# Optimization experiments

Measured on AMD Instinct MI355X. Metric: run time of the kernel, lower is better.

## Reference

```python
import jax, jax.numpy as jnp
import numpy as np

H = 64
N_BENE, N_DIAG, N_TREAT = 200000, 10000, 100000
E = 1000000
N_INST = 500000

def setup_inputs() -> dict:
    key = jax.random.key(0)
    ks = jax.random.split(key, 24)
    def lin(k, din, dout):
        kw, kb = jax.random.split(k)
        s = 1.0 / np.sqrt(din)
        return (jax.random.uniform(kw, (din, dout), jnp.float32, -s, s),
                jax.random.uniform(kb, (dout,), jnp.float32, -s, s))
    inp = {
        'bene_ids': jax.random.randint(ks[0], (N_BENE,), 0, 10000, jnp.int32),
        'diag_ids': jax.random.randint(ks[1], (N_DIAG,), 0, 200, jnp.int32),
        'treatment_ids': jax.random.randint(ks[2], (N_TREAT,), 0, 1000, jnp.int32),
        'b2d_src': jax.random.randint(ks[3], (E,), 0, N_BENE, jnp.int32),
        'b2d_dst': jax.random.randint(ks[4], (E,), 0, N_DIAG, jnp.int32),
        't2d_src': jax.random.randint(ks[5], (E,), 0, N_TREAT, jnp.int32),
        't2d_dst': jax.random.randint(ks[6], (E,), 0, N_DIAG, jnp.int32),
        'inst2type': jax.random.randint(ks[7], (N_INST,), 0, N_DIAG, jnp.int32),
        'bene_emb': jax.random.normal(ks[8], (10000, H), jnp.float32),
        'diag_emb': jax.random.normal(ks[9], (200, H), jnp.float32),
        'treat_emb': jax.random.normal(ks[10], (1000, H), jnp.float32),
    }
    # two conv layers: msg_bene_to_diag (Wb,bb), msg_treatment_to_diag (Wt,bt), update_diag (Wu,bu)
    names = ['Wb0','bb0','Wt0','bt0','Wu0','bu0','Wb1','bb1','Wt1','bt1','Wu1','bu1']
    idx = 11
    for i in range(0, len(names), 2):
        W, b = lin(ks[idx], H, H); idx += 1
        inp[names[i]] = W; inp[names[i+1]] = b
    inp['oW1'], inp['ob1'] = lin(ks[idx], H, H // 2); idx += 1
    inp['oW2'], inp['ob2'] = lin(ks[idx], H // 2, 1)
    return inp

def _conv(bene, diag, treat, b2d_src, b2d_dst, t2d_src, t2d_dst, Wb, bb, Wt, bt, Wu, bu):
    msg_b = bene[b2d_src] @ Wb + bb                      # [E, H]
    agg_b = jax.ops.segment_sum(msg_b, b2d_dst, num_segments=N_DIAG)
    msg_t = treat[t2d_src] @ Wt + bt                     # [E, H]
    agg_t = jax.ops.segment_sum(msg_t, t2d_dst, num_segments=N_DIAG)
    combined = 0.5 * (agg_b + agg_t)                     # mean over 2 message types
    return combined @ Wu + bu

def reference(bene_ids, diag_ids, treatment_ids, b2d_src, b2d_dst, t2d_src, t2d_dst,
              inst2type, bene_emb, diag_emb, treat_emb,
              Wb0, bb0, Wt0, bt0, Wu0, bu0, Wb1, bb1, Wt1, bt1, Wu1, bu1,
              oW1, ob1, oW2, ob2):
    bene = bene_emb[bene_ids]
    diag = diag_emb[diag_ids]
    treat = treat_emb[treatment_ids]
    for (Wb, bb, Wt, bt, Wu, bu) in ((Wb0, bb0, Wt0, bt0, Wu0, bu0),
                                     (Wb1, bb1, Wt1, bt1, Wu1, bu1)):
        diag = _conv(bene, diag, treat, b2d_src, b2d_dst, t2d_src, t2d_dst,
                     Wb, bb, Wt, bt, Wu, bu)
        bene, diag, treat = jax.nn.relu(bene), jax.nn.relu(diag), jax.nn.relu(treat)
    inst = diag[inst2type]                               # [N_INST, H]
    h = jax.nn.relu(inst @ oW1 + ob1)                    # dropout is eval-mode identity
    return jax.nn.sigmoid(h @ oW2 + ob2)[:, 0]
```

## Files before the change

### kernel.cpp

```cpp
#include <hip/hip_runtime.h>
#include <hip/hip_bf16.h>

#define Hdim 64
#define NDIAG 10000
#define NEDGE 1000000
#define NINST 500000
#define NBENE_EMB 10000
#define NTREAT_EMB 1000

#define NSUP 79
#define SSHIFT 7
#define SMASK 127
#define NROWS (NSUP * 128)
#define CAP_S 13568
#define BUFK 64
#define EPB 2048
#define NSPB 489
#define NSPLIT 8
#define FPSCALE 1048576.0f
#define FPINV (1.0f / 1048576.0f)

__global__ __launch_bounds__(512) void split_prep_kernel(
    const int* __restrict__ b2d_dst, const int* __restrict__ b2d_src, const int* __restrict__ bene_ids,
    const int* __restrict__ t2d_dst, const int* __restrict__ t2d_src, const int* __restrict__ treat_ids,
    const float* __restrict__ bene_emb, const float* __restrict__ treat_emb,
    int* __restrict__ itab_b, int* __restrict__ itab_t,
    int* __restrict__ gcur_b, int* __restrict__ gbuf_b,
    int* __restrict__ gcur_t, int* __restrict__ gbuf_t,
    int* __restrict__ iacc, int* __restrict__ degs) {
    const int ty = blockIdx.y;
    const int tid = threadIdx.x;

    if (ty == 2) {
        int gid = blockIdx.x * 512 + tid;
        const int gstride = NSPB * 512;
        int4 z4 = {0, 0, 0, 0};
        int4* i4 = (int4*)iacc;
        for (int i = gid; i < 2 * NROWS * 16; i += gstride) i4[i] = z4;
        for (int i = gid; i < 2 * NROWS; i += gstride) degs[i] = 0;
        for (int i = gid; i < NBENE_EMB * Hdim; i += gstride)
            itab_b[i] = (int)(fmaxf(bene_emb[i], 0.f) * FPSCALE);
        for (int i = gid; i < NTREAT_EMB * Hdim; i += gstride)
            itab_t[i] = (int)(fmaxf(treat_emb[i], 0.f) * FPSCALE);
        return;
    }

    const int* dst  = ty ? t2d_dst  : b2d_dst;
    const int* src  = ty ? t2d_src  : b2d_src;
    const int* ids  = ty ? treat_ids: bene_ids;
    int* gcur = ty ? gcur_t : gcur_b;
    int* gbuf = ty ? gbuf_t : gbuf_b;

    __shared__ int buf[BUFK][NSUP];
    __shared__ int cnt[NSUP];
    __shared__ int base_s[NSUP];
    for (int i = tid; i < NSUP; i += 512) cnt[i] = 0;
    __syncthreads();

    const int e4 = blockIdx.x * EPB + tid * 4;
    if (e4 < NEDGE) {
        int4 d4 = *reinterpret_cast<const int4*>(dst + e4);
        int4 s4 = *reinterpret_cast<const int4*>(src + e4);
        int dd[4] = {d4.x, d4.y, d4.z, d4.w};
        int ss[4] = {s4.x, s4.y, s4.z, s4.w};
        int cc[4];
        #pragma unroll
        for (int u = 0; u < 4; ++u) cc[u] = ids[ss[u]];
        #pragma unroll
        for (int u = 0; u < 4; ++u) {
            int b = dd[u] >> SSHIFT;
            int v = ((dd[u] & SMASK) << 16) | cc[u];
            int p = atomicAdd(&cnt[b], 1);
            if (p < BUFK) {
                buf[p][b] = v;
            } else {
                int gp = atomicAdd(&gcur[b], 1);
                if (gp < CAP_S) gbuf[b * CAP_S + gp] = v;
            }
        }
    }
    __syncthreads();

    const int wid = tid >> 6, lane = tid & 63;
    if (wid < 2) {
        int b = (wid << 6) + lane;
        if (b < NSUP) {
            int n = min(cnt[b], BUFK);
            base_s[b] = atomicAdd(&gcur[b], n);
        }
    }
    __syncthreads();

    for (int b = wid; b < NSUP; b += 8) {
        int n = min(cnt[b], BUFK);
        int gp0 = base_s[b];
        if (lane < n) {
            int gp = gp0 + lane;
            if (gp < CAP_S) gbuf[b * CAP_S + gp] = buf[lane][b];
        }
    }
}

__global__ __launch_bounds__(512) void agg_kernel(
    const int* __restrict__ gbuf_b, const int* __restrict__ gcur_b, const int* __restrict__ itab_b,
    const int* __restrict__ gbuf_t, const int* __restrict__ gcur_t, const int* __restrict__ itab_t,
    int* __restrict__ iacc, int* __restrict__ degs) {
    const int bk = blockIdx.x, ty = blockIdx.y, sp = blockIdx.z;
    const int* gbuf = ty ? gbuf_t : gbuf_b;
    const int* gcur = ty ? gcur_t : gcur_b;
    const int* itab = ty ? itab_t : itab_b;
    int* iac = iacc + (size_t)ty * NROWS * Hdim;
    int* dg  = degs + ty * NROWS;

    __shared__ int acc[128][64];
    __shared__ int dhist[128];

    const int tid = threadIdx.x;
    const int wid = tid >> 6, lane = tid & 63;
    int4* a4 = (int4*)&acc[0][0];
    for (int i = tid; i < 2048; i += 512) a4[i] = int4{0, 0, 0, 0};
    if (tid < 128) dhist[tid] = 0;
    __syncthreads();

    const int count = min(gcur[bk], CAP_S);
    const int slice = (count + NSPLIT - 1) / NSPLIT;
    const int s0 = sp * slice;
    const int s1 = min(count, s0 + slice);
    const int n = max(0, s1 - s0);
    const int nfull = n >> 6;
    const int rem = n & 63;
    const int* bucket = gbuf + bk * CAP_S;

    for (int ck = wid; ck < nfull; ck += 8) {
        int vv = bucket[s0 + (ck << 6) + lane];
        atomicAdd(&dhist[(vv >> 16) & SMASK], 1);
        #pragma unroll
        for (int g = 0; g < 8; ++g) {
            int dla[8], iv[8];
            #pragma unroll
            for (int u = 0; u < 8; ++u) {
                int s = __builtin_amdgcn_readlane(vv, g * 8 + u);
                dla[u] = (s >> 16) & SMASK;
                iv[u] = itab[(s & 0xffff) * Hdim + lane];
            }
            #pragma unroll
            for (int u = 0; u < 8; ++u)
                atomicAdd(&acc[dla[u]][lane], iv[u]);
        }
    }
    if (rem && wid == (nfull & 7)) {
        int base2 = s0 + (nfull << 6);
        int vv = (lane < rem) ? bucket[base2 + lane] : 0;
        if (lane < rem) atomicAdd(&dhist[(vv >> 16) & SMASK], 1);
        for (int u = 0; u < rem; ++u) {
            int s = __builtin_amdgcn_readlane(vv, u);
            atomicAdd(&acc[(s >> 16) & SMASK][lane], itab[(s & 0xffff) * Hdim + lane]);
        }
    }
    __syncthreads();

    for (int i = wid; i < 128; i += 8)
        atomicAdd(&iac[(size_t)((bk << 7) + i) * Hdim + lane], acc[i][lane]);
    if (tid < 128) {
        int t = dhist[tid];
        if (t) atomicAdd(&dg[(bk << 7) + tid], t);
    }
}

__global__ __launch_bounds__(256) void head_kernel(
    const int* __restrict__ iacc, const int* __restrict__ degs,
    const float* __restrict__ Wb1, const float* __restrict__ bb1,
    const float* __restrict__ Wt1, const float* __restrict__ bt1,
    const float* __restrict__ Wu1, const float* __restrict__ bu1,
    const float* __restrict__ oW1, const float* __restrict__ ob1,
    const float* __restrict__ oW2, const float* __restrict__ ob2,
    float* __restrict__ per_diag_out) {
    int wave = threadIdx.x >> 6;
    int lane = threadIdx.x & 63;
    int d = blockIdx.x * 4 + wave;

    __shared__ float Sb[4][64];
    __shared__ float St[4][64];
    __shared__ float Cc[4][64];
    __shared__ float Dd[4][64];

    int sbi = iacc[(size_t)d * Hdim + lane];
    int sti = iacc[(size_t)(NROWS + d) * Hdim + lane];
    int dgb = degs[d];
    int dgt = degs[NROWS + d];
    Sb[wave][lane] = (float)sbi * FPINV;
    St[wave][lane] = (float)sti * FPINV;
    __syncthreads();

    float ab = (float)dgb * bb1[lane];
    float at = (float)dgt * bt1[lane];
    #pragma unroll 8
    for (int l = 0; l < Hdim; ++l) {
        ab += Sb[wave][l] * Wb1[l * Hdim + lane];
        at += St[wave][l] * Wt1[l * Hdim + lane];
    }
    float comb = 0.5f * (ab + at);
    Cc[wave][lane] = comb;
    __syncthreads();

    float dg = bu1[lane];
    #pragma unroll 8
    for (int l = 0; l < Hdim; ++l) dg += Cc[wave][l] * Wu1[l * Hdim + lane];
    float d1 = fmaxf(dg, 0.f);
    Dd[wave][lane] = d1;
    __syncthreads();

    float contrib = 0.f;
    if (lane < 32) {
        float h = ob1[lane];
        #pragma unroll 8
        for (int l = 0; l < Hdim; ++l) h += Dd[wave][l] * oW1[l * 32 + lane];
        h = fmaxf(h, 0.f);
        contrib = h * oW2[lane];
    }
    for (int o = 32; o > 0; o >>= 1) contrib += __shfl_down(contrib, o);
    if (lane == 0) {
        float logit = contrib + ob2[0];
        per_diag_out[d] = 1.f / (1.f + __expf(-logit));
    }
}

__global__ void gather_kernel(const int* __restrict__ inst2type,
                              const float* __restrict__ per_diag_out,
                              float* __restrict__ out) {
    int i = blockIdx.x * blockDim.x + threadIdx.x;
    int i4 = i * 4;
    if (i4 >= NINST) return;
    int4 t = *reinterpret_cast<const int4*>(inst2type + i4);
    float4 r;
    r.x = per_diag_out[t.x];
    r.y = per_diag_out[t.y];
    r.z = per_diag_out[t.z];
    r.w = per_diag_out[t.w];
    *reinterpret_cast<float4*>(out + i4) = r;
}

extern "C" void kernel_launch(void* const* d_in, const int* in_sizes, int n_in,
                              void* d_out, int out_size, void* d_ws, size_t ws_size,
                              hipStream_t stream) {
    (void)in_sizes; (void)n_in; (void)out_size; (void)ws_size;

    const int*   bene_ids  = (const int*)d_in[0];
    const int*   treat_ids = (const int*)d_in[2];
    const int*   b2d_src   = (const int*)d_in[3];
    const int*   b2d_dst   = (const int*)d_in[4];
    const int*   t2d_src   = (const int*)d_in[5];
    const int*   t2d_dst   = (const int*)d_in[6];
    const int*   inst2type = (const int*)d_in[7];
    const float* bene_emb  = (const float*)d_in[8];
    const float* treat_emb = (const float*)d_in[10];
    const float* Wb1 = (const float*)d_in[17];
    const float* bb1 = (const float*)d_in[18];
    const float* Wt1 = (const float*)d_in[19];
    const float* bt1 = (const float*)d_in[20];
    const float* Wu1 = (const float*)d_in[21];
    const float* bu1 = (const float*)d_in[22];
    const float* oW1 = (const float*)d_in[23];
    const float* ob1 = (const float*)d_in[24];
    const float* oW2 = (const float*)d_in[25];
    const float* ob2 = (const float*)d_in[26];
    float* out = (float*)d_out;

    char* w = (char*)d_ws;
    auto alloc = [&](size_t bytes) {
        char* p = w;
        w += (bytes + 255) & ~(size_t)255;
        return p;
    };
    int* gcur_all = (int*)alloc(2 * NSUP * 4);
    int* gcur_b = gcur_all;
    int* gcur_t = gcur_all + NSUP;
    int* gbuf_b = (int*)alloc((size_t)NSUP * CAP_S * 4);
    int* gbuf_t = (int*)alloc((size_t)NSUP * CAP_S * 4);
    int* itab_b = (int*)alloc((size_t)NBENE_EMB * Hdim * 4);
    int* itab_t = (int*)alloc((size_t)NTREAT_EMB * Hdim * 4);
    int* iacc   = (int*)alloc((size_t)2 * NROWS * Hdim * 4);
    int* degs   = (int*)alloc((size_t)2 * NROWS * 4);
    float* pdo  = (float*)alloc(NDIAG * 4);

    hipMemsetAsync(gcur_all, 0, 2 * NSUP * 4, stream);

    split_prep_kernel<<<dim3(NSPB, 3), 512, 0, stream>>>(
        b2d_dst, b2d_src, bene_ids, t2d_dst, t2d_src, treat_ids,
        bene_emb, treat_emb, itab_b, itab_t,
        gcur_b, gbuf_b, gcur_t, gbuf_t, iacc, degs);

    agg_kernel<<<dim3(NSUP, 2, NSPLIT), 512, 0, stream>>>(
        gbuf_b, gcur_b, itab_b, gbuf_t, gcur_t, itab_t, iacc, degs);

    head_kernel<<<NDIAG / 4, 256, 0, stream>>>(
        iacc, degs,
        Wb1, bb1, Wt1, bt1, Wu1, bu1, oW1, ob1, oW2, ob2, pdo);

    gather_kernel<<<(NINST / 4 + 255) / 256, 256, 0, stream>>>(inst2type, pdo, out);
}
```

Measured before the change: 215.8 us.

## Quantize embedding tables to 16-bit, prefetch bucket chunks, batch head over 5 diags per wave

The embedding lookup tables become 16-bit fixed point with a 4096 scale instead of 32-bit with a 2^20 scale. This halves the gather traffic in the aggregation kernel, at the cost of coarser quantization of the accumulated sums. The aggregation loop now software-prefetches the next bucket chunk and issues 16 gathers per group instead of 8. The head kernel is restructured to stage all weights in LDS and compute 5 diagnoses per wave using readlane broadcasts, with fewer, larger blocks.

```diff
diff --git a/kernel.cpp b/kernel.cpp
--- a/kernel.cpp
+++ b/kernel.cpp
@@ -17,14 +17,14 @@
 #define EPB 2048
 #define NSPB 489
 #define NSPLIT 8
-#define FPSCALE 1048576.0f
-#define FPINV (1.0f / 1048576.0f)
+#define QSCALE 4096.0f
+#define QINV (1.0f / 4096.0f)
 
 __global__ __launch_bounds__(512) void split_prep_kernel(
     const int* __restrict__ b2d_dst, const int* __restrict__ b2d_src, const int* __restrict__ bene_ids,
     const int* __restrict__ t2d_dst, const int* __restrict__ t2d_src, const int* __restrict__ treat_ids,
     const float* __restrict__ bene_emb, const float* __restrict__ treat_emb,
-    int* __restrict__ itab_b, int* __restrict__ itab_t,
+    unsigned short* __restrict__ itab_b, unsigned short* __restrict__ itab_t,
     int* __restrict__ gcur_b, int* __restrict__ gbuf_b,
     int* __restrict__ gcur_t, int* __restrict__ gbuf_t,
     int* __restrict__ iacc, int* __restrict__ degs) {
@@ -39,9 +39,9 @@
         for (int i = gid; i < 2 * NROWS * 16; i += gstride) i4[i] = z4;
         for (int i = gid; i < 2 * NROWS; i += gstride) degs[i] = 0;
         for (int i = gid; i < NBENE_EMB * Hdim; i += gstride)
-            itab_b[i] = (int)(fmaxf(bene_emb[i], 0.f) * FPSCALE);
+            itab_b[i] = (unsigned short)(fmaxf(bene_emb[i], 0.f) * QSCALE + 0.5f);
         for (int i = gid; i < NTREAT_EMB * Hdim; i += gstride)
-            itab_t[i] = (int)(fmaxf(treat_emb[i], 0.f) * FPSCALE);
+            itab_t[i] = (unsigned short)(fmaxf(treat_emb[i], 0.f) * QSCALE + 0.5f);
         return;
     }
 
@@ -102,13 +102,13 @@
 }
 
 __global__ __launch_bounds__(512) void agg_kernel(
-    const int* __restrict__ gbuf_b, const int* __restrict__ gcur_b, const int* __restrict__ itab_b,
-    const int* __restrict__ gbuf_t, const int* __restrict__ gcur_t, const int* __restrict__ itab_t,
+    const int* __restrict__ gbuf_b, const int* __restrict__ gcur_b, const unsigned short* __restrict__ itab_b,
+    const int* __restrict__ gbuf_t, const int* __restrict__ gcur_t, const unsigned short* __restrict__ itab_t,
     int* __restrict__ iacc, int* __restrict__ degs) {
     const int bk = blockIdx.x, ty = blockIdx.y, sp = blockIdx.z;
     const int* gbuf = ty ? gbuf_t : gbuf_b;
     const int* gcur = ty ? gcur_t : gcur_b;
-    const int* itab = ty ? itab_t : itab_b;
+    const unsigned short* itab = ty ? itab_t : itab_b;
     int* iac = iacc + (size_t)ty * NROWS * Hdim;
     int* dg  = degs + ty * NROWS;
 
@@ -131,30 +131,34 @@
     const int rem = n & 63;
     const int* bucket = gbuf + bk * CAP_S;
 
-    for (int ck = wid; ck < nfull; ck += 8) {
-        int vv = bucket[s0 + (ck << 6) + lane];
+    int ck = wid;
+    int vv = (ck < nfull) ? bucket[s0 + (ck << 6) + lane] : 0;
+    while (ck < nfull) {
+        int nk = ck + 8;
+        int vn = (nk < nfull) ? bucket[s0 + (nk << 6) + lane] : 0;
         atomicAdd(&dhist[(vv >> 16) & SMASK], 1);
         #pragma unroll
-        for (int g = 0; g < 8; ++g) {
-            int dla[8], iv[8];
+        for (int g = 0; g < 4; ++g) {
+            int dla[16], iv[16];
             #pragma unroll
-            for (int u = 0; u < 8; ++u) {
-                int s = __builtin_amdgcn_readlane(vv, g * 8 + u);
+            for (int u = 0; u < 16; ++u) {
+                int s = __builtin_amdgcn_readlane(vv, g * 16 + u);
                 dla[u] = (s >> 16) & SMASK;
-                iv[u] = itab[(s & 0xffff) * Hdim + lane];
+                iv[u] = (int)itab[(s & 0xffff) * Hdim + lane];
             }
             #pragma unroll
-            for (int u = 0; u < 8; ++u)
+            for (int u = 0; u < 16; ++u)
                 atomicAdd(&acc[dla[u]][lane], iv[u]);
         }
+        vv = vn; ck = nk;
     }
     if (rem && wid == (nfull & 7)) {
         int base2 = s0 + (nfull << 6);
-        int vv = (lane < rem) ? bucket[base2 + lane] : 0;
-        if (lane < rem) atomicAdd(&dhist[(vv >> 16) & SMASK], 1);
+        int vr = (lane < rem) ? bucket[base2 + lane] : 0;
+        if (lane < rem) atomicAdd(&dhist[(vr >> 16) & SMASK], 1);
         for (int u = 0; u < rem; ++u) {
-            int s = __builtin_amdgcn_readlane(vv, u);
-            atomicAdd(&acc[(s >> 16) & SMASK][lane], itab[(s & 0xffff) * Hdim + lane]);
+            int s = __builtin_amdgcn_readlane(vr, u);
+            atomicAdd(&acc[(s >> 16) & SMASK][lane], (int)itab[(s & 0xffff) * Hdim + lane]);
         }
     }
     __syncthreads();
@@ -167,7 +171,7 @@
     }
 }
 
-__global__ __launch_bounds__(256) void head_kernel(
+__global__ __launch_bounds__(512) void head_kernel(
     const int* __restrict__ iacc, const int* __restrict__ degs,
     const float* __restrict__ Wb1, const float* __restrict__ bb1,
     const float* __restrict__ Wt1, const float* __restrict__ bt1,
@@ -175,53 +179,78 @@
     const float* __restrict__ oW1, const float* __restrict__ ob1,
     const float* __restrict__ oW2, const float* __restrict__ ob2,
     float* __restrict__ per_diag_out) {
-    int wave = threadIdx.x >> 6;
-    int lane = threadIdx.x & 63;
-    int d = blockIdx.x * 4 + wave;
-
-    __shared__ float Sb[4][64];
-    __shared__ float St[4][64];
-    __shared__ float Cc[4][64];
-    __shared__ float Dd[4][64];
-
-    int sbi = iacc[(size_t)d * Hdim + lane];
-    int sti = iacc[(size_t)(NROWS + d) * Hdim + lane];
-    int dgb = degs[d];
-    int dgt = degs[NROWS + d];
-    Sb[wave][lane] = (float)sbi * FPINV;
-    St[wave][lane] = (float)sti * FPINV;
-    __syncthreads();
-
-    float ab = (float)dgb * bb1[lane];
-    float at = (float)dgt * bt1[lane];
-    #pragma unroll 8
+    __shared__ float Ws[14336];
+    const int tid = threadIdx.x;
+    for (int i = tid; i < 4096; i += 512) {
+        Ws[i]        = Wb1[i];
+        Ws[4096 + i] = Wt1[i];
+        Ws[8192 + i] = Wu1[i];
+    }
+    for (int i = tid; i < 2048; i += 512) Ws[12288 + i] = oW1[i];
+    __syncthreads();
+    const float* Wb1s = Ws;
+    const float* Wt1s = Ws + 4096;
+    const float* Wu1s = Ws + 8192;
+    const float* oW1s = Ws + 12288;
+
+    const int wid = tid >> 6, lane = tid & 63;
+    const int d0 = blockIdx.x * 40 + wid * 5;
+
+    float sb[5], st[5], ab[5], at[5];
+    #pragma unroll
+    for (int nn = 0; nn < 5; ++nn) {
+        int d = d0 + nn;
+        sb[nn] = (float)iacc[(size_t)d * Hdim + lane] * QINV;
+        st[nn] = (float)iacc[(size_t)(NROWS + d) * Hdim + lane] * QINV;
+        ab[nn] = (float)degs[d] * bb1[lane];
+        at[nn] = (float)degs[NROWS + d] * bt1[lane];
+    }
     for (int l = 0; l < Hdim; ++l) {
-        ab += Sb[wave][l] * Wb1[l * Hdim + lane];
-        at += St[wave][l] * Wt1[l * Hdim + lane];
-    }
-    float comb = 0.5f * (ab + at);
-    Cc[wave][lane] = comb;
-    __syncthreads();
-
-    float dg = bu1[lane];
-    #pragma unroll 8
-    for (int l = 0; l < Hdim; ++l) dg += Cc[wave][l] * Wu1[l * Hdim + lane];
-    float d1 = fmaxf(dg, 0.f);
-    Dd[wave][lane] = d1;
-    __syncthreads();
-
-    float contrib = 0.f;
-    if (lane < 32) {
-        float h = ob1[lane];
-        #pragma unroll 8
-        for (int l = 0; l < Hdim; ++l) h += Dd[wave][l] * oW1[l * 32 + lane];
-        h = fmaxf(h, 0.f);
-        contrib = h * oW2[lane];
-    }
-    for (int o = 32; o > 0; o >>= 1) contrib += __shfl_down(contrib, o);
-    if (lane == 0) {
-        float logit = contrib + ob2[0];
-        per_diag_out[d] = 1.f / (1.f + __expf(-logit));
+        float wb = Wb1s[l * 64 + lane];
+        float wt = Wt1s[l * 64 + lane];
+        #pragma unroll
+        for (int nn = 0; nn < 5; ++nn) {
+            ab[nn] += __uint_as_float(__builtin_amdgcn_readlane(__float_as_uint(sb[nn]), l)) * wb;
+            at[nn] += __uint_as_float(__builtin_amdgcn_readlane(__float_as_uint(st[nn]), l)) * wt;
+        }
+    }
+    float cb[5];
+    #pragma unroll
+    for (int nn = 0; nn < 5; ++nn) cb[nn] = 0.5f * (ab[nn] + at[nn]);
+
+    float dgv[5];
+    #pragma unroll
+    for (int nn = 0; nn < 5; ++nn) dgv[nn] = bu1[lane];
+    for (int l = 0; l < Hdim; ++l) {
+        float wu = Wu1s[l * 64 + lane];
+        #pragma unroll
+        for (int nn = 0; nn < 5; ++nn)
+            dgv[nn] += __uint_as_float(__builtin_amdgcn_readlane(__float_as_uint(cb[nn]), l)) * wu;
+    }
+    float d1[5];
+    #pragma unroll
+    for (int nn = 0; nn < 5; ++nn) d1[nn] = fmaxf(dgv[nn], 0.f);
+
+    float ob1v = (lane < 32) ? ob1[lane] : 0.f;
+    float ow2v = (lane < 32) ? oW2[lane] : 0.f;
+    float ob2v = ob2[0];
+    float h[5];
+    #pragma unroll
+    for (int nn = 0; nn < 5; ++nn) h[nn] = ob1v;
+    for (int l = 0; l < Hdim; ++l) {
+        float wo = oW1s[l * 32 + (lane & 31)];
+        #pragma unroll
+        for (int nn = 0; nn < 5; ++nn)
+            h[nn] += __uint_as_float(__builtin_amdgcn_readlane(__float_as_uint(d1[nn]), l)) * wo;
+    }
+    #pragma unroll
+    for (int nn = 0; nn < 5; ++nn) {
+        float c = fmaxf(h[nn], 0.f) * ow2v;
+        for (int o = 32; o > 0; o >>= 1) c += __shfl_down(c, o);
+        if (lane == 0) {
+            float logit = c + ob2v;
+            per_diag_out[d0 + nn] = 1.f / (1.f + __expf(-logit));
+        }
     }
 }
 
@@ -277,8 +306,8 @@
     int* gcur_t = gcur_all + NSUP;
     int* gbuf_b = (int*)alloc((size_t)NSUP * CAP_S * 4);
     int* gbuf_t = (int*)alloc((size_t)NSUP * CAP_S * 4);
-    int* itab_b = (int*)alloc((size_t)NBENE_EMB * Hdim * 4);
-    int* itab_t = (int*)alloc((size_t)NTREAT_EMB * Hdim * 4);
+    unsigned short* itab_b = (unsigned short*)alloc((size_t)NBENE_EMB * Hdim * 2);
+    unsigned short* itab_t = (unsigned short*)alloc((size_t)NTREAT_EMB * Hdim * 2);
     int* iacc   = (int*)alloc((size_t)2 * NROWS * Hdim * 4);
     int* degs   = (int*)alloc((size_t)2 * NROWS * 4);
     float* pdo  = (float*)alloc(NDIAG * 4);
@@ -293,7 +322,7 @@
     agg_kernel<<<dim3(NSUP, 2, NSPLIT), 512, 0, stream>>>(
         gbuf_b, gcur_b, itab_b, gbuf_t, gcur_t, itab_t, iacc, degs);
 
-    head_kernel<<<NDIAG / 4, 256, 0, stream>>>(
+    head_kernel<<<250, 512, 0, stream>>>(
         iacc, degs,
         Wb1, bb1, Wt1, bt1, Wu1, bu1, oW1, ob1, oW2, ob2, pdo);
 
```

Measured after the change: 207.0 us. 1.04x faster.
